# Kernel optimization log

Hardware: AMD Instinct MI355X
Metric: run time of the kernel (lower is better)

Reference implementation:

```python
import jax, jax.numpy as jnp
import numpy as np

B, H, HKV, D, DV, S, M, BN = 16, 32, 8, 128, 128, 8192, 64, 64


def setup_inputs() -> dict:
    key = jax.random.key(0)
    k1, k2, k3, k4 = jax.random.split(key, 4)
    query = jax.random.normal(k1, (B, H, D), dtype=jnp.float32)
    K = jax.random.normal(k2, (B, S, HKV, D), dtype=jnp.float32)
    V = jax.random.normal(k3, (B, S, HKV, DV), dtype=jnp.float32)
    # selected KV block ids per (batch, kv_head); -1 would mean 'skip block'
    block_indices = jax.random.randint(k4, (B, HKV, M), 0, S // BN).astype(jnp.int32)
    cache_seqlens = jnp.full((B,), S, dtype=jnp.int32)
    return {"query": query, "key": K, "value": V,
            "block_indices": block_indices, "cache_seqlens": cache_seqlens,
            "block_size": BN}


def reference(query, key, value, block_indices, cache_seqlens, block_size):
    # query: [B,H,D]  key: [B,S,HKV,D]  value: [B,S,HKV,DV]
    # block_indices: [B,HKV,M] int32 (-1 = invalid)  cache_seqlens: [B] int32
    Bb, Hh, Dd = query.shape
    _, Ss, Hkv, Dv = value.shape
    G = Hh // Hkv  # GQA group size
    scale = 1.0 / np.sqrt(Dd).astype(np.float32)

    valid_blk = block_indices >= 0                              # [B,HKV,M]
    idx = jnp.where(valid_blk, block_indices, 0)
    pos4 = idx[..., None] * block_size + jnp.arange(block_size)  # [B,HKV,M,bn]
    mask4 = valid_blk[..., None] & (pos4 < cache_seqlens[:, None, None, None])
    pos = pos4.reshape(Bb, Hkv, -1)                              # [B,HKV,N] N=M*bn
    mask = mask4.reshape(Bb, Hkv, -1)

    # gather selected KV blocks per (batch, kv_head)
    Kt = key.transpose(0, 2, 1, 3)    # [B,HKV,S,D]
    Vt = value.transpose(0, 2, 1, 3)  # [B,HKV,S,DV]
    Kg = jnp.take_along_axis(Kt, pos[..., None], axis=2)  # [B,HKV,N,D]
    Vg = jnp.take_along_axis(Vt, pos[..., None], axis=2)  # [B,HKV,N,DV]

    q = query.reshape(Bb, Hkv, G, Dd)                      # [B,HKV,G,D]
    s = jnp.einsum('bhgd,bhnd->bhgn', q, Kg) * scale       # [B,HKV,G,N]
    s = jnp.where(mask[:, :, None, :], s, -jnp.inf)
    p = jax.nn.softmax(s, axis=-1)                         # online-softmax equiv.
    o = jnp.einsum('bhgn,bhnd->bhgd', p, Vg)               # [B,HKV,G,DV]
    return o.reshape(Bb, Hh, Dv)
```

## Files before the change

### kernel.cpp

```cpp
#include <hip/hip_runtime.h>
#include <math.h>

#define B_    16
#define H_    32
#define HKV_  8
#define G_    4
#define D_    128
#define DV_   128
#define S_    8192
#define M_    64
#define BN_   64
#define KVSTRIDE (HKV_ * D_)

#define CHUNK_ 16
#define NBPW_  8
#define SPLIT_ (M_ / NBPW_)
#define NCTOT_ (NBPW_ * BN_ / CHUNK_)

__device__ __forceinline__ void gload_lds16(const float* gsrc, float* lds_dst) {
    __builtin_amdgcn_global_load_lds(
        (const __attribute__((address_space(1))) void*)gsrc,
        (__attribute__((address_space(3))) void*)lds_dst,
        16, 0, 0);
}

__device__ __forceinline__ float bcast_lane(float v, int srclane) {
    return __uint_as_float(__builtin_amdgcn_readlane(__float_as_uint(v), srclane));
}

__global__ __launch_bounds__(256)
void sfa_partial(const float* __restrict__ q,
                 const float* __restrict__ K,
                 const float* __restrict__ V,
                 const int*   __restrict__ blk_idx,
                 const int*   __restrict__ seqlens,
                 float* __restrict__ o_ws,
                 float* __restrict__ ml_ws)
{
    __shared__ float Klds[2][CHUNK_ * D_];
    __shared__ float Vlds[2][CHUNK_ * DV_];

    const int w    = blockIdx.x;
    const int hkv  = w & 7;
    const int t    = w >> 3;
    const int b    = t & 15;
    const int oct  = t >> 4;
    const int bh   = b * HKV_ + hkv;

    const int tid  = threadIdx.x;
    const int wave = tid >> 6;
    const int lane = tid & 63;
    const int c    = lane & 3;
    const int jr   = lane >> 2;

    const int h = hkv * G_ + wave;
    const float kscale = 0.08838834764831845f * 1.4426950408889634f;

    float4 q4[8];
    {
        const float* qp = q + (size_t)(b * H_ + h) * D_ + c * 4;
        #pragma unroll
        for (int f = 0; f < 8; ++f) {
            float4 tq = *(const float4*)(qp + f * 16);
            q4[f] = make_float4(tq.x * kscale, tq.y * kscale,
                                tq.z * kscale, tq.w * kscale);
        }
    }

    int vblk = 0;
    if (lane < NBPW_) vblk = blk_idx[bh * M_ + oct * NBPW_ + lane];

    const int seqlen = seqlens[b];
    const float* Kb = K + (size_t)b * S_ * KVSTRIDE + hkv * D_;
    const float* Vb = V + (size_t)b * S_ * KVSTRIDE + hkv * D_;

    asm volatile("s_waitcnt vmcnt(0)" ::: "memory");

    auto stageK = [&](int cc, int blk) {
        const int blkc = (blk < 0) ? 0 : blk;
        const size_t rowbase = (size_t)blkc * BN_ + (cc & 3) * CHUNK_;
        float* dst = &Klds[cc & 1][0];
        #pragma unroll
        for (int i = 0; i < 2; ++i) {
            const int p   = wave * 2 + i;
            const int row = 2 * p + (lane >> 5);
            const int g16 = lane & 31;
            const float* src = Kb + (rowbase + row) * KVSTRIDE
                                  + ((g16 ^ (row & 7)) << 2);
            gload_lds16(src, dst + p * 256);
        }
    };
    auto stageV = [&](int cc, int blk) {
        const int blkc = (blk < 0) ? 0 : blk;
        const size_t rowbase = (size_t)blkc * BN_ + (cc & 3) * CHUNK_;
        float* dst = &Vlds[cc & 1][0];
        #pragma unroll
        for (int i = 0; i < 2; ++i) {
            const int p   = wave * 2 + i;
            const int row = 2 * p + (lane >> 5);
            const int g16 = lane & 31;
            const float* src = Vb + (rowbase + row) * KVSTRIDE + (g16 << 2);
            gload_lds16(src, dst + p * 256);
        }
    };
    auto blkOf = [&](int cc) -> int {
        return __builtin_amdgcn_readlane(vblk, cc >> 2);
    };

    float m  = -INFINITY;
    float l  = 0.f;
    float o0 = 0.f, o1 = 0.f;

    stageK(0, blkOf(0));
    stageV(0, blkOf(0));
    stageK(1, blkOf(1));

    #pragma unroll 2
    for (int cc = 0; cc < NCTOT_; ++cc) {
        const int  blk  = blkOf(cc);
        const bool bval = (blk >= 0);
        const int  pos0 = ((blk < 0) ? 0 : blk) * BN_ + (cc & 3) * CHUNK_;
        const bool last = (cc == NCTOT_ - 1);

        if (last) asm volatile("s_waitcnt vmcnt(2)" ::: "memory");
        else      asm volatile("s_waitcnt vmcnt(4)" ::: "memory");
        __builtin_amdgcn_s_barrier();
        __builtin_amdgcn_sched_barrier(0);

        float s0;
        {
            const float* kr = &Klds[cc & 1][jr * D_];
            float acc = 0.f;
            #pragma unroll
            for (int f = 0; f < 8; ++f) {
                const int gg = (((f * 4 + c) ^ (jr & 7)) << 2);
                float4 k4 = *(const float4*)(kr + gg);
                acc += q4[f].x * k4.x;
                acc += q4[f].y * k4.y;
                acc += q4[f].z * k4.z;
                acc += q4[f].w * k4.w;
            }
            acc += __shfl_xor(acc, 1);
            acc += __shfl_xor(acc, 2);
            s0 = (bval && (pos0 + jr) < seqlen) ? acc : -INFINITY;
        }

        if (cc + 1 < NCTOT_) stageV(cc + 1, blkOf(cc + 1));

        if (last) asm volatile("s_waitcnt vmcnt(0)" ::: "memory");
        else      asm volatile("s_waitcnt vmcnt(4)" ::: "memory");
        __builtin_amdgcn_s_barrier();
        __builtin_amdgcn_sched_barrier(0);

        if (cc + 2 < NCTOT_) stageK(cc + 2, blkOf(cc + 2));

        float bmax = s0;
        #pragma unroll
        for (int off = 4; off < 64; off <<= 1)
            bmax = fmaxf(bmax, __shfl_xor(bmax, off));

        const float newm = fmaxf(m, bmax);
        if (newm != -INFINITY) {
            const float rr = __builtin_amdgcn_exp2f(m - newm);
            const float p0 = __builtin_amdgcn_exp2f(s0 - newm);
            float ps = p0;
            #pragma unroll
            for (int off = 4; off < 64; off <<= 1)
                ps += __shfl_xor(ps, off);

            l  = l * rr + ps;
            o0 *= rr;
            o1 *= rr;
            m  = newm;

            const float* vp0 = &Vlds[cc & 1][lane * 2];
            #pragma unroll
            for (int jj = 0; jj < 16; ++jj) {
                const float pj = bcast_lane(p0, jj * 4);
                const float2 v2 = *(const float2*)(vp0 + jj * DV_);
                o0 += pj * v2.x;
                o1 += pj * v2.y;
            }
        }
    }

    const int pidx = (bh * G_ + wave) * SPLIT_ + oct;
    *(float2*)(o_ws + (size_t)pidx * DV_ + lane * 2) = make_float2(o0, o1);
    if (lane == 0)
        *(float2*)(ml_ws + pidx * 2) = make_float2(m, l);
}

template<int SPLIT>
__global__ __launch_bounds__(64)
void sfa_reduce(const float* __restrict__ o_ws,
                const float* __restrict__ ml_ws,
                float* __restrict__ out)
{
    const int bhg  = blockIdx.x;
    const int lane = threadIdx.x;

    float mi = -INFINITY, li = 0.f;
    if (lane < SPLIT) {
        const float2 t = ((const float2*)ml_ws)[bhg * SPLIT + lane];
        mi = t.x; li = t.y;
    }
    float mfull = mi;
    #pragma unroll
    for (int off = 1; off < 64; off <<= 1)
        mfull = fmaxf(mfull, __shfl_xor(mfull, off));

    const float f = (mi == -INFINITY) ? 0.f
                  : __builtin_amdgcn_exp2f(mi - mfull);
    float L = li * f;
    #pragma unroll
    for (int off = 1; off < 64; off <<= 1)
        L += __shfl_xor(L, off);

    float o0 = 0.f, o1 = 0.f;
    #pragma unroll
    for (int i = 0; i < SPLIT; ++i) {
        const float fi = bcast_lane(f, i);
        if (fi != 0.f) {
            const float* op = o_ws + (size_t)(bhg * SPLIT + i) * DV_ + lane * 2;
            o0 += fi * op[0];
            o1 += fi * op[1];
        }
    }
    const float inv = (L > 0.f) ? (1.f / L) : 0.f;
    out[(size_t)bhg * DV_ + lane * 2]     = o0 * inv;
    out[(size_t)bhg * DV_ + lane * 2 + 1] = o1 * inv;
}

extern "C" void kernel_launch(void* const* d_in, const int* in_sizes, int n_in,
                              void* d_out, int out_size, void* d_ws, size_t ws_size,
                              hipStream_t stream) {
    const float* q    = (const float*)d_in[0];
    const float* K    = (const float*)d_in[1];
    const float* V    = (const float*)d_in[2];
    const int*   bidx = (const int*)d_in[3];
    const int*   slen = (const int*)d_in[4];

    float* o_ws  = (float*)d_ws;
    float* ml_ws = o_ws + (size_t)B_ * HKV_ * G_ * SPLIT_ * DV_;

    sfa_partial<<<B_ * HKV_ * SPLIT_, 256, 0, stream>>>(
        q, K, V, bidx, slen, o_ws, ml_ws);

    sfa_reduce<SPLIT_><<<B_ * H_, 64, 0, stream>>>(o_ws, ml_ws, (float*)d_out);
}
```

Measured before the change: 88.74 us.

## Fuse split-KV reduction into partial kernel via last-block atomic counter

Merges the separate reduce kernel into the partial kernel. Each block bumps a per-(batch,kv-head) atomic counter after writing its partial output, and the last block to arrive combines all splits and writes the final output. This removes the second kernel launch and its dependency gap, but adds a hipMemsetAsync to clear the counters, thread fences, and volatile reads in the tail of the last block.

```diff
diff --git a/kernel.cpp b/kernel.cpp
--- a/kernel.cpp
+++ b/kernel.cpp
@@ -29,16 +29,19 @@
 }
 
 __global__ __launch_bounds__(256)
-void sfa_partial(const float* __restrict__ q,
-                 const float* __restrict__ K,
-                 const float* __restrict__ V,
-                 const int*   __restrict__ blk_idx,
-                 const int*   __restrict__ seqlens,
-                 float* __restrict__ o_ws,
-                 float* __restrict__ ml_ws)
+void sfa_fused(const float* __restrict__ q,
+               const float* __restrict__ K,
+               const float* __restrict__ V,
+               const int*   __restrict__ blk_idx,
+               const int*   __restrict__ seqlens,
+               float* __restrict__ o_ws,
+               float* __restrict__ ml_ws,
+               int*   __restrict__ cnt,
+               float* __restrict__ out)
 {
     __shared__ float Klds[2][CHUNK_ * D_];
     __shared__ float Vlds[2][CHUNK_ * DV_];
+    __shared__ int   s_old;
 
     const int w    = blockIdx.x;
     const int hkv  = w & 7;
@@ -188,47 +191,45 @@
     *(float2*)(o_ws + (size_t)pidx * DV_ + lane * 2) = make_float2(o0, o1);
     if (lane == 0)
         *(float2*)(ml_ws + pidx * 2) = make_float2(m, l);
-}
-
-template<int SPLIT>
-__global__ __launch_bounds__(64)
-void sfa_reduce(const float* __restrict__ o_ws,
-                const float* __restrict__ ml_ws,
-                float* __restrict__ out)
-{
-    const int bhg  = blockIdx.x;
-    const int lane = threadIdx.x;
+
+    __threadfence();
+    if (tid == 0) s_old = atomicAdd(&cnt[bh], 1);
+    __syncthreads();
+    if (s_old != SPLIT_ - 1) return;
+    __threadfence();
 
     float mi = -INFINITY, li = 0.f;
-    if (lane < SPLIT) {
-        const float2 t = ((const float2*)ml_ws)[bhg * SPLIT + lane];
-        mi = t.x; li = t.y;
+    if (lane < SPLIT_) {
+        const volatile float* mlp = ml_ws + ((bh * G_ + wave) * SPLIT_ + lane) * 2;
+        mi = mlp[0];
+        li = mlp[1];
     }
     float mfull = mi;
     #pragma unroll
     for (int off = 1; off < 64; off <<= 1)
         mfull = fmaxf(mfull, __shfl_xor(mfull, off));
 
-    const float f = (mi == -INFINITY) ? 0.f
-                  : __builtin_amdgcn_exp2f(mi - mfull);
-    float L = li * f;
+    const float fct = (mi == -INFINITY) ? 0.f
+                    : __builtin_amdgcn_exp2f(mi - mfull);
+    float L = li * fct;
     #pragma unroll
     for (int off = 1; off < 64; off <<= 1)
         L += __shfl_xor(L, off);
 
-    float o0 = 0.f, o1 = 0.f;
+    float r0 = 0.f, r1 = 0.f;
     #pragma unroll
-    for (int i = 0; i < SPLIT; ++i) {
-        const float fi = bcast_lane(f, i);
+    for (int i = 0; i < SPLIT_; ++i) {
+        const float fi = bcast_lane(fct, i);
         if (fi != 0.f) {
-            const float* op = o_ws + (size_t)(bhg * SPLIT + i) * DV_ + lane * 2;
-            o0 += fi * op[0];
-            o1 += fi * op[1];
+            const volatile float* op =
+                o_ws + (size_t)((bh * G_ + wave) * SPLIT_ + i) * DV_ + lane * 2;
+            r0 += fi * op[0];
+            r1 += fi * op[1];
         }
     }
     const float inv = (L > 0.f) ? (1.f / L) : 0.f;
-    out[(size_t)bhg * DV_ + lane * 2]     = o0 * inv;
-    out[(size_t)bhg * DV_ + lane * 2 + 1] = o1 * inv;
+    *(float2*)(out + (size_t)(b * H_ + h) * DV_ + lane * 2) =
+        make_float2(r0 * inv, r1 * inv);
 }
 
 extern "C" void kernel_launch(void* const* d_in, const int* in_sizes, int n_in,
@@ -242,9 +243,10 @@
 
     float* o_ws  = (float*)d_ws;
     float* ml_ws = o_ws + (size_t)B_ * HKV_ * G_ * SPLIT_ * DV_;
-
-    sfa_partial<<<B_ * HKV_ * SPLIT_, 256, 0, stream>>>(
-        q, K, V, bidx, slen, o_ws, ml_ws);
-
-    sfa_reduce<SPLIT_><<<B_ * H_, 64, 0, stream>>>(o_ws, ml_ws, (float*)d_out);
-}
+    int*   cnt   = (int*)(ml_ws + (size_t)B_ * HKV_ * G_ * SPLIT_ * 2);
+
+    hipMemsetAsync(cnt, 0, B_ * HKV_ * sizeof(int), stream);
+
+    sfa_fused<<<B_ * HKV_ * SPLIT_, 256, 0, stream>>>(
+        q, K, V, bidx, slen, o_ws, ml_ws, cnt, (float*)d_out);
+}
```

Result: slower. 254.1 us (+186.4%).

## Deduplicate selected KV block indices and weight softmax by multiplicity

Applied to the files above, without the earlier changes.

A new small kernel removes repeated block ids per (batch, kv_head) and records each id's multiplicity. The partial kernel then loads each unique block only once and scales its softmax probabilities by the multiplicity, which preserves the reference result exactly. This cuts redundant K/V memory traffic when indices repeat. In exchange it adds a kernel launch, uneven work across the split blocks, and a dynamic loop bound that replaces the previous fixed, partly unrolled loop.

```diff
diff --git a/kernel.cpp b/kernel.cpp
--- a/kernel.cpp
+++ b/kernel.cpp
@@ -13,9 +13,7 @@
 #define KVSTRIDE (HKV_ * D_)
 
 #define CHUNK_ 16
-#define NBPW_  8
-#define SPLIT_ (M_ / NBPW_)
-#define NCTOT_ (NBPW_ * BN_ / CHUNK_)
+#define SPLIT_ 8
 
 __device__ __forceinline__ void gload_lds16(const float* gsrc, float* lds_dst) {
     __builtin_amdgcn_global_load_lds(
@@ -28,11 +26,37 @@
     return __uint_as_float(__builtin_amdgcn_readlane(__float_as_uint(v), srclane));
 }
 
+__global__ __launch_bounds__(64)
+void sfa_dedup(const int* __restrict__ blk_idx,
+               int2* __restrict__ dlist,
+               int*  __restrict__ dcnt)
+{
+    const int gidx = blockIdx.x;
+    const int lane = threadIdx.x;
+    const int id   = blk_idx[gidx * M_ + lane];
+
+    int  mult  = 0;
+    bool first = (id >= 0);
+    #pragma unroll
+    for (int j = 0; j < 64; ++j) {
+        const int idj = __builtin_amdgcn_readlane(id, j);
+        if (idj == id) {
+            ++mult;
+            if (j < lane) first = false;
+        }
+    }
+    const unsigned long long mask = __ballot(first);
+    const int pos = __popcll(mask & ((1ull << lane) - 1ull));
+    if (first) dlist[gidx * M_ + pos] = make_int2(id, mult);
+    if (lane == 0) dcnt[gidx] = (int)__popcll(mask);
+}
+
 __global__ __launch_bounds__(256)
 void sfa_partial(const float* __restrict__ q,
                  const float* __restrict__ K,
                  const float* __restrict__ V,
-                 const int*   __restrict__ blk_idx,
+                 const int2*  __restrict__ dlist,
+                 const int*   __restrict__ dcnt,
                  const int*   __restrict__ seqlens,
                  float* __restrict__ o_ws,
                  float* __restrict__ ml_ws)
@@ -67,18 +91,36 @@
         }
     }
 
-    int vblk = 0;
-    if (lane < NBPW_) vblk = blk_idx[bh * M_ + oct * NBPW_ + lane];
-
+    const int dc   = dcnt[bh];
+    const int nblk = (dc > oct) ? (((dc - 1 - oct) >> 3) + 1) : 0;
+
+    const int pidx = (bh * G_ + wave) * SPLIT_ + oct;
+    if (nblk == 0) {
+        *(float2*)(o_ws + (size_t)pidx * DV_ + lane * 2) = make_float2(0.f, 0.f);
+        if (lane == 0) *(float2*)(ml_ws + pidx * 2) = make_float2(-INFINITY, 0.f);
+        return;
+    }
+
+    int   vid   = 0;
+    float vmulf = 0.f;
+    if (lane < nblk) {
+        const int2 e = dlist[bh * M_ + oct + 8 * lane];
+        vid   = e.x;
+        vmulf = (float)e.y;
+    }
+
+    const int NCT = nblk * 4;
     const int seqlen = seqlens[b];
     const float* Kb = K + (size_t)b * S_ * KVSTRIDE + hkv * D_;
     const float* Vb = V + (size_t)b * S_ * KVSTRIDE + hkv * D_;
 
     asm volatile("s_waitcnt vmcnt(0)" ::: "memory");
 
-    auto stageK = [&](int cc, int blk) {
-        const int blkc = (blk < 0) ? 0 : blk;
-        const size_t rowbase = (size_t)blkc * BN_ + (cc & 3) * CHUNK_;
+    auto blkOf = [&](int cc) -> int {
+        return __builtin_amdgcn_readlane(vid, cc >> 2);
+    };
+    auto stageK = [&](int cc) {
+        const size_t rowbase = (size_t)blkOf(cc) * BN_ + (cc & 3) * CHUNK_;
         float* dst = &Klds[cc & 1][0];
         #pragma unroll
         for (int i = 0; i < 2; ++i) {
@@ -90,9 +132,8 @@
             gload_lds16(src, dst + p * 256);
         }
     };
-    auto stageV = [&](int cc, int blk) {
-        const int blkc = (blk < 0) ? 0 : blk;
-        const size_t rowbase = (size_t)blkc * BN_ + (cc & 3) * CHUNK_;
+    auto stageV = [&](int cc) {
+        const size_t rowbase = (size_t)blkOf(cc) * BN_ + (cc & 3) * CHUNK_;
         float* dst = &Vlds[cc & 1][0];
         #pragma unroll
         for (int i = 0; i < 2; ++i) {
@@ -103,24 +144,18 @@
             gload_lds16(src, dst + p * 256);
         }
     };
-    auto blkOf = [&](int cc) -> int {
-        return __builtin_amdgcn_readlane(vblk, cc >> 2);
-    };
 
     float m  = -INFINITY;
     float l  = 0.f;
     float o0 = 0.f, o1 = 0.f;
 
-    stageK(0, blkOf(0));
-    stageV(0, blkOf(0));
-    stageK(1, blkOf(1));
-
-    #pragma unroll 2
-    for (int cc = 0; cc < NCTOT_; ++cc) {
-        const int  blk  = blkOf(cc);
-        const bool bval = (blk >= 0);
-        const int  pos0 = ((blk < 0) ? 0 : blk) * BN_ + (cc & 3) * CHUNK_;
-        const bool last = (cc == NCTOT_ - 1);
+    stageK(0); stageV(0); stageK(1);
+
+    #pragma unroll 1
+    for (int cc = 0; cc < NCT; ++cc) {
+        const int  pos0 = blkOf(cc) * BN_ + (cc & 3) * CHUNK_;
+        const bool last = (cc == NCT - 1);
+        const float wc  = bcast_lane(vmulf, cc >> 2);
 
         if (last) asm volatile("s_waitcnt vmcnt(2)" ::: "memory");
         else      asm volatile("s_waitcnt vmcnt(4)" ::: "memory");
@@ -142,17 +177,17 @@
             }
             acc += __shfl_xor(acc, 1);
             acc += __shfl_xor(acc, 2);
-            s0 = (bval && (pos0 + jr) < seqlen) ? acc : -INFINITY;
-        }
-
-        if (cc + 1 < NCTOT_) stageV(cc + 1, blkOf(cc + 1));
+            s0 = ((pos0 + jr) < seqlen) ? acc : -INFINITY;
+        }
+
+        if (cc + 1 < NCT) stageV(cc + 1);
 
         if (last) asm volatile("s_waitcnt vmcnt(0)" ::: "memory");
         else      asm volatile("s_waitcnt vmcnt(4)" ::: "memory");
         __builtin_amdgcn_s_barrier();
         __builtin_amdgcn_sched_barrier(0);
 
-        if (cc + 2 < NCTOT_) stageK(cc + 2, blkOf(cc + 2));
+        if (cc + 2 < NCT) stageK(cc + 2);
 
         float bmax = s0;
         #pragma unroll
@@ -162,7 +197,7 @@
         const float newm = fmaxf(m, bmax);
         if (newm != -INFINITY) {
             const float rr = __builtin_amdgcn_exp2f(m - newm);
-            const float p0 = __builtin_amdgcn_exp2f(s0 - newm);
+            const float p0 = wc * __builtin_amdgcn_exp2f(s0 - newm);
             float ps = p0;
             #pragma unroll
             for (int off = 4; off < 64; off <<= 1)
@@ -184,7 +219,6 @@
         }
     }
 
-    const int pidx = (bh * G_ + wave) * SPLIT_ + oct;
     *(float2*)(o_ws + (size_t)pidx * DV_ + lane * 2) = make_float2(o0, o1);
     if (lane == 0)
         *(float2*)(ml_ws + pidx * 2) = make_float2(m, l);
@@ -242,9 +276,13 @@
 
     float* o_ws  = (float*)d_ws;
     float* ml_ws = o_ws + (size_t)B_ * HKV_ * G_ * SPLIT_ * DV_;
+    int2*  dlist = (int2*)(ml_ws + (size_t)B_ * HKV_ * G_ * SPLIT_ * 2);
+    int*   dcnt  = (int*)(dlist + (size_t)B_ * HKV_ * M_);
+
+    sfa_dedup<<<B_ * HKV_, 64, 0, stream>>>(bidx, dlist, dcnt);
 
     sfa_partial<<<B_ * HKV_ * SPLIT_, 256, 0, stream>>>(
-        q, K, V, bidx, slen, o_ws, ml_ws);
+        q, K, V, dlist, dcnt, slen, o_ws, ml_ws);
 
     sfa_reduce<SPLIT_><<<B_ * H_, 64, 0, stream>>>(o_ws, ml_ws, (float*)d_out);
 }
```

Result: slower. 92.13 us (+3.8%).
